# Kernel tuning notes

Hardware: AMD Instinct MI355X
Metric: run time of the kernel (lower is better)

Reference implementation:

```python
import jax, jax.numpy as jnp
import numpy as np

B, N, C = 32, 197, 768
H = 12
D = C // H
NUM_CLASSES = 100
SCALE = D ** -0.5


def setup_inputs() -> dict:
    key = jax.random.key(0)
    ks = jax.random.split(key, 8)
    x = jax.random.normal(ks[0], (B, N, C), dtype=jnp.float32)
    y = jax.random.randint(ks[1], (B,), 0, NUM_CLASSES, dtype=jnp.int32)
    qkv_w = jax.random.normal(ks[2], (3 * C, C), dtype=jnp.float32) * 0.02
    qkv_b = jax.random.normal(ks[3], (3 * C,), dtype=jnp.float32) * 0.02
    proj_w = jax.random.normal(ks[4], (C, C), dtype=jnp.float32) * 0.02
    proj_b = jax.random.normal(ks[5], (C,), dtype=jnp.float32) * 0.02
    mask_attn = jnp.ones((NUM_CLASSES, H, D), jnp.float32) + 0.1 * jax.random.normal(ks[6], (NUM_CLASSES, H, D), dtype=jnp.float32)
    mask_proj = jnp.ones((NUM_CLASSES, C, C), jnp.float32) + 0.1 * jax.random.normal(ks[7], (NUM_CLASSES, C, C), dtype=jnp.float32)
    return {"x": x, "y": y, "qkv_w": qkv_w, "qkv_b": qkv_b,
            "proj_w": proj_w, "proj_b": proj_b,
            "mask_attn": mask_attn, "mask_proj": mask_proj}


def reference(x, y, qkv_w, qkv_b, proj_w, proj_b, mask_attn, mask_proj):
    b, n, c = x.shape
    # qkv projection: (B,N,3C) -> (3,B,H,N,D)
    qkv = (x @ qkv_w.T + qkv_b).reshape(b, n, 3, H, D).transpose(2, 0, 3, 1, 4)
    q, k, v = qkv[0], qkv[1], qkv[2]
    a = jnp.einsum('bhnd,bhmd->bhnm', q * SCALE, k)
    a = jax.nn.softmax(a, axis=-1)  # attn_drop is identity in eval
    o = jnp.einsum('bhnm,bhmd->bhnd', a, v)
    # per-class attention mask: (B,H,1,D)
    o = o * mask_attn[y][:, :, None, :]
    o = o.transpose(0, 2, 1, 3).reshape(b, n, c)
    # per-sample masked projection weight: (B, out, in)
    W = proj_w[None, :, :] * mask_proj[y]
    out = jnp.einsum('bni,boi->bno', o, W) + proj_b[None, None, :]
    return out  # proj_drop is identity in eval
```

## Files before the change

kernel.cpp:

```cpp
#include <hip/hip_runtime.h>

typedef unsigned short u16;
typedef __attribute__((ext_vector_type(8))) short short8;
typedef __attribute__((ext_vector_type(4))) short s16x4;
typedef __attribute__((ext_vector_type(4))) float f32x4;
typedef __attribute__((ext_vector_type(4))) u16 u16x4;

#define GPTR(p) ((const __attribute__((address_space(1))) void*)(p))
#define LPTR(p) ((__attribute__((address_space(3))) void*)(p))

#if __has_builtin(__builtin_amdgcn_mfma_f32_16x16x16bf16_1k)
#define MFMA16x16(a, b, c) __builtin_amdgcn_mfma_f32_16x16x16bf16_1k(a, b, c, 0, 0, 0)
#elif __has_builtin(__builtin_amdgcn_mfma_f32_16x16x16_bf16)
#define MFMA16x16(a, b, c) __builtin_amdgcn_mfma_f32_16x16x16_bf16(a, b, c, 0, 0, 0)
#else
__host__ __device__ static inline f32x4 MFMA16x16_host_stub(s16x4, s16x4, f32x4 c) { return c; }
#define MFMA16x16(a, b, c) MFMA16x16_host_stub(a, b, c)
#endif

__device__ __forceinline__ u16 f2bf(float f) {
    union { float f; unsigned u; } a; a.f = f;
    unsigned r = a.u + 0x7FFFu + ((a.u >> 16) & 1u);
    return (u16)(r >> 16);
}

__global__ __launch_bounds__(256) void cvt_fused_kernel(const float* __restrict__ xin,
                                                        const float* __restrict__ win,
                                                        u16* __restrict__ xout,
                                                        u16* __restrict__ wout) {
    int i = (blockIdx.x * 256 + threadIdx.x) * 4;
    const float* src;
    u16* dst;
    int j;
    if (i < 4841472) {
        src = xin; dst = xout; j = i;
    } else {
        src = win; dst = wout; j = i - 4841472;
    }
    f32x4 v = *(const f32x4*)(src + j);
    u16x4 o;
#pragma unroll
    for (int k = 0; k < 4; ++k) o[k] = f2bf(v[k]);
    *(u16x4*)(dst + j) = o;
}

__global__ __launch_bounds__(512, 2) void qkv_gemm_kernel(
    const u16* __restrict__ A,
    const u16* __restrict__ Bm,
    const float* __restrict__ bias,
    u16* __restrict__ qb, u16* __restrict__ kb, u16* __restrict__ vb) {
    __shared__ __align__(16) u16 As[2][256 * 64];
    __shared__ __align__(16) u16 Bs[2][256 * 64];
    const int tid = threadIdx.x;
    const int w = tid >> 6, l = tid & 63;
    const int wy = w >> 2, wx = w & 3;
    const int dl = l & 15, g4 = l >> 4;
    const int fr = (dl & 7) << 4;

    const int wg = blockIdx.x;
    const int xcd = wg & 7, pos = wg >> 3;
    const int id2 = (xcd < 1 ? xcd * 29 : 29 + (xcd - 1) * 28) + pos;
    const int bm = id2 / 9, bn = id2 % 9;

    f32x4 acc[8][4] = {};

#define QKV_STAGE(bi, kt)                                                                   \
    {                                                                                       \
        _Pragma("unroll")                                                                   \
        for (int cc = 0; cc < 4; ++cc) {                                                    \
            int c = w * 256 + cc * 64 + l;                                                  \
            int row = c >> 3;                                                               \
            int cs = ((c & 7) << 4) ^ ((row & 7) << 4);                                     \
            __builtin_amdgcn_global_load_lds(                                               \
                GPTR((const char*)(A + (size_t)(bm * 256 + row) * 768 + (kt)) + cs),        \
                LPTR((char*)As[bi] + c * 16), 16, 0, 0);                                    \
            __builtin_amdgcn_global_load_lds(                                               \
                GPTR((const char*)(Bm + (size_t)(bn * 256 + row) * 768 + (kt)) + cs),       \
                LPTR((char*)Bs[bi] + c * 16), 16, 0, 0);                                    \
        }                                                                                   \
    }

    QKV_STAGE(0, 0)
    __syncthreads();
    int cur = 0;
#pragma unroll 1
    for (int t = 0; t < 12; ++t) {
        if (t < 11) QKV_STAGE(cur ^ 1, (t + 1) * 64)
#pragma unroll
        for (int s = 0; s < 2; ++s) {
            const int ce = ((s << 6) | (g4 << 4)) ^ fr;
            short8 af[8], bf[4];
#pragma unroll
            for (int mi = 0; mi < 8; ++mi)
                af[mi] = *(const short8*)((const char*)As[cur] + (wy * 128 + mi * 16 + dl) * 128 + ce);
#pragma unroll
            for (int ni = 0; ni < 4; ++ni)
                bf[ni] = *(const short8*)((const char*)Bs[cur] + (wx * 64 + ni * 16 + dl) * 128 + ce);
#pragma unroll
            for (int mi = 0; mi < 8; ++mi)
#pragma unroll
                for (int ni = 0; ni < 4; ++ni)
                    acc[mi][ni] = __builtin_amdgcn_mfma_f32_16x16x32_bf16(af[mi], bf[ni], acc[mi][ni], 0, 0, 0);
        }
        __syncthreads();
        cur ^= 1;
    }
#undef QKV_STAGE

#pragma unroll
    for (int ni = 0; ni < 4; ++ni) {
        int col = bn * 256 + wx * 64 + ni * 16 + dl;
        int s = (col >= 1536) ? 2 : (col >= 768) ? 1 : 0;
        int j = col - s * 768;
        int h = j >> 6, d = j & 63;
        float bv = bias[col];
        u16* dst = (s == 0) ? qb : (s == 1) ? kb : vb;
        float sc = (s == 0) ? 0.125f : 1.0f;
#pragma unroll
        for (int mi = 0; mi < 8; ++mi) {
#pragma unroll
            for (int r = 0; r < 4; ++r) {
                int row = bm * 256 + wy * 128 + mi * 16 + g4 * 4 + r;
                if (row < 6304) {
                    int bi = row / 197;
                    int n = row - bi * 197;
                    dst[((size_t)(bi * 12 + h) * 197 + n) * 64 + d] = f2bf((acc[mi][ni][r] + bv) * sc);
                }
            }
        }
    }
}

#define VPAD 212
__global__ __launch_bounds__(512) void attn_kernel(
    const u16* __restrict__ qg_all, const u16* __restrict__ kg_all, const u16* __restrict__ vg_all,
    const int* __restrict__ y, const float* __restrict__ mask_attn,
    u16* __restrict__ omid) {
    __shared__ __align__(16) u16 Ks[208 * 64];
    __shared__ __align__(16) u16 Vst[64 * VPAD];
    const int bh = blockIdx.x >> 1, half = blockIdx.x & 1;
    const int b = bh / 12, h = bh % 12;
    const int tid = threadIdx.x, w = tid >> 6, l = tid & 63;
    const int dl = l & 15, g = l >> 4;
    const size_t base = (size_t)bh * 197 * 64;
    const u16* qg = qg_all + base;
    const u16* kg = kg_all + base;
    const u16* vg = vg_all + base;
    const short8 zero8 = {0, 0, 0, 0, 0, 0, 0, 0};
    const int ycls = y[b];

    for (int c = tid; c < 208 * 8; c += 512) {
        int row = c >> 3, colb = (c & 7) * 16;
        short8 val = zero8;
        if (row < 197) val = *(const short8*)(kg + row * 64 + (c & 7) * 8);
        int bo = (row * 128 + colb) ^ ((row & 7) << 4);
        *(short8*)((char*)Ks + bo) = val;
    }
    for (int c = tid; c < 208 * 8; c += 512) {
        int row = c >> 3, col = (c & 7) * 8;
        short8 val = zero8;
        if (row < 197) val = *(const short8*)(vg + row * 64 + col);
#pragma unroll
        for (int j = 0; j < 8; ++j) Vst[(col + j) * VPAD + row] = (u16)val[j];
    }
    __syncthreads();

    const int ci_end = half ? 13 : 7;
    for (int ci = half * 7 + w; ci < ci_end; ci += 8) {
        int qrow = ci * 16 + dl;
        const u16* qr = qg + (size_t)qrow * 64 + g * 8;
        short8 q0 = *(const short8*)(qr);
        short8 q1 = *(const short8*)(qr + 32);

        f32x4 sc[13];
#pragma unroll
        for (int jb = 0; jb < 13; ++jb) {
            int krow = jb * 16 + dl;
            int sw = (krow & 7) << 4;
            short8 k0 = *(const short8*)((const char*)Ks + ((krow * 128 + g * 16) ^ sw));
            short8 k1 = *(const short8*)((const char*)Ks + ((krow * 128 + 64 + g * 16) ^ sw));
            f32x4 t = {0.f, 0.f, 0.f, 0.f};
            t = __builtin_amdgcn_mfma_f32_16x16x32_bf16(k0, q0, t, 0, 0, 0);
            t = __builtin_amdgcn_mfma_f32_16x16x32_bf16(k1, q1, t, 0, 0, 0);
            sc[jb] = t;
        }
#pragma unroll
        for (int r = 0; r < 4; ++r)
            if (192 + g * 4 + r >= 197) sc[12][r] = -1e30f;

        float mx = -1e30f;
#pragma unroll
        for (int jb = 0; jb < 13; ++jb)
#pragma unroll
            for (int r = 0; r < 4; ++r) mx = fmaxf(mx, sc[jb][r]);
        mx = fmaxf(mx, __shfl_xor(mx, 16));
        mx = fmaxf(mx, __shfl_xor(mx, 32));
        float ssum = 0.f;
#pragma unroll
        for (int jb = 0; jb < 13; ++jb)
#pragma unroll
            for (int r = 0; r < 4; ++r) {
                float e = __expf(sc[jb][r] - mx);
                sc[jb][r] = e;
                ssum += e;
            }
        ssum += __shfl_xor(ssum, 16);
        ssum += __shfl_xor(ssum, 32);
        float inv = 1.0f / ssum;

        s16x4 pb[13];
#pragma unroll
        for (int jb = 0; jb < 13; ++jb) {
            s16x4 pv;
#pragma unroll
            for (int r = 0; r < 4; ++r) pv[r] = (short)f2bf(sc[jb][r] * inv);
            pb[jb] = pv;
        }

#pragma unroll
        for (int db = 0; db < 4; ++db) {
            f32x4 o = {0.f, 0.f, 0.f, 0.f};
#pragma unroll
            for (int jb = 0; jb < 13; ++jb) {
                s16x4 va = *(const s16x4*)&Vst[(db * 16 + dl) * VPAD + jb * 16 + g * 4];
                o = MFMA16x16(va, pb[jb], o);
            }
            if (qrow < 197) {
                int d = db * 16 + g * 4;
                f32x4 mv = *(const f32x4*)(mask_attn + ((size_t)ycls * 12 + h) * 64 + d);
                u16x4 ov;
#pragma unroll
                for (int r = 0; r < 4; ++r) ov[r] = f2bf(o[r] * mv[r]);
                *(u16x4*)(omid + ((size_t)(b * 256 + qrow)) * 768 + h * 64 + d) = ov;
            }
        }
    }
}

__global__ __launch_bounds__(512, 2) void proj_gemm_kernel(
    const u16* __restrict__ A,
    const float* __restrict__ proj_w,
    const float* __restrict__ mask_proj,
    const int* __restrict__ y,
    const float* __restrict__ bias,
    float* __restrict__ out) {
    __shared__ __align__(16) u16 Ap[2][256 * 64];
    __shared__ __align__(16) u16 Bp[2][128 * 64];
    const int tid = threadIdx.x;
    const int w = tid >> 6, l = tid & 63;
    const int wy = w >> 1, wx = w & 1;
    const int dl = l & 15, g4 = l >> 4;
    const int fr = (dl & 7) << 4;

    const int wg = blockIdx.x;
    const int id2 = (wg & 7) * 24 + (wg >> 3);
    const int b = id2 / 6, bn = id2 % 6;
    const size_t mbase = (size_t)y[b] * 589824;

    const int brow = tid >> 2;
    const int becol = (tid & 3) * 16;
    const int bcb = becol * 2;
    const int bsw = (brow & 7) << 4;

    f32x4 pw[4], pm[4];

#define PROJ_LOADB(kt)                                                              \
    {                                                                               \
        size_t off = (size_t)(bn * 128 + brow) * 768 + (kt) + becol;                \
        _Pragma("unroll")                                                           \
        for (int j = 0; j < 4; ++j) {                                               \
            pw[j] = *(const f32x4*)(proj_w + off + j * 4);                          \
            pm[j] = *(const f32x4*)(mask_proj + mbase + off + j * 4);               \
        }                                                                           \
    }

#define PROJ_WRITEB(bi)                                                             \
    {                                                                               \
        short8 o0, o1;                                                              \
        _Pragma("unroll")                                                           \
        for (int j = 0; j < 4; ++j) {                                               \
            o0[j] = (short)f2bf(pw[0][j] * pm[0][j]);                               \
            o0[4 + j] = (short)f2bf(pw[1][j] * pm[1][j]);                           \
            o1[j] = (short)f2bf(pw[2][j] * pm[2][j]);                               \
            o1[4 + j] = (short)f2bf(pw[3][j] * pm[3][j]);                           \
        }                                                                           \
        char* bp = (char*)Bp[bi] + brow * 128;                                      \
        *(short8*)(bp + (bcb ^ bsw)) = o0;                                          \
        *(short8*)(bp + ((bcb + 16) ^ bsw)) = o1;                                   \
    }

#define PROJ_STAGEA(bi, kt)                                                         \
    {                                                                               \
        _Pragma("unroll")                                                           \
        for (int cc = 0; cc < 4; ++cc) {                                            \
            int c = w * 256 + cc * 64 + l;                                          \
            int row = c >> 3;                                                       \
            int cs = ((c & 7) << 4) ^ ((row & 7) << 4);                             \
            __builtin_amdgcn_global_load_lds(                                       \
                GPTR((const char*)(A + (size_t)(b * 256 + row) * 768 + (kt)) + cs), \
                LPTR((char*)Ap[bi] + c * 16), 16, 0, 0);                            \
        }                                                                           \
    }

    f32x4 acc[4][4] = {};
    PROJ_LOADB(0)
    PROJ_STAGEA(0, 0)
    PROJ_WRITEB(0)
    __syncthreads();
    int cur = 0;
#pragma unroll 1
    for (int t = 0; t < 12; ++t) {
        if (t < 11) {
            PROJ_STAGEA(cur ^ 1, (t + 1) * 64)
            PROJ_LOADB((t + 1) * 64)
        }
#pragma unroll
        for (int s = 0; s < 2; ++s) {
            const int ce = ((s << 6) | (g4 << 4)) ^ fr;
            short8 af[4], bf[4];
#pragma unroll
            for (int mi = 0; mi < 4; ++mi)
                af[mi] = *(const short8*)((const char*)Ap[cur] + (wy * 64 + mi * 16 + dl) * 128 + ce);
#pragma unroll
            for (int ni = 0; ni < 4; ++ni)
                bf[ni] = *(const short8*)((const char*)Bp[cur] + (wx * 64 + ni * 16 + dl) * 128 + ce);
#pragma unroll
            for (int mi = 0; mi < 4; ++mi)
#pragma unroll
                for (int ni = 0; ni < 4; ++ni)
                    acc[mi][ni] = __builtin_amdgcn_mfma_f32_16x16x32_bf16(af[mi], bf[ni], acc[mi][ni], 0, 0, 0);
        }
        if (t < 11) PROJ_WRITEB(cur ^ 1)
        __syncthreads();
        cur ^= 1;
    }

#pragma unroll
    for (int ni = 0; ni < 4; ++ni) {
        int col = bn * 128 + wx * 64 + ni * 16 + dl;
        float bv = bias[col];
#pragma unroll
        for (int mi = 0; mi < 4; ++mi) {
#pragma unroll
            for (int r = 0; r < 4; ++r) {
                int row = wy * 64 + mi * 16 + g4 * 4 + r;
                if (row < 197)
                    out[((size_t)b * 197 + row) * 768 + col] = acc[mi][ni][r] + bv;
            }
        }
    }
#undef PROJ_LOADB
#undef PROJ_WRITEB
#undef PROJ_STAGEA
}

extern "C" void kernel_launch(void* const* d_in, const int* in_sizes, int n_in,
                              void* d_out, int out_size, void* d_ws, size_t ws_size,
                              hipStream_t stream) {
    const float* x = (const float*)d_in[0];
    const int* y = (const int*)d_in[1];
    const float* qkv_w = (const float*)d_in[2];
    const float* qkv_b = (const float*)d_in[3];
    const float* proj_w = (const float*)d_in[4];
    const float* proj_b = (const float*)d_in[5];
    const float* mask_attn = (const float*)d_in[6];
    const float* mask_proj = (const float*)d_in[7];
    float* out = (float*)d_out;

    u16* xb = (u16*)d_ws;
    u16* wqkvb = xb + (size_t)6400 * 768;
    u16* qb = wqkvb + (size_t)2304 * 768;
    u16* kb = qb + (size_t)76288 * 64;
    u16* vb = kb + (size_t)76288 * 64;
    u16* omid = vb + (size_t)76288 * 64;

    cvt_fused_kernel<<<6456, 256, 0, stream>>>(x, qkv_w, xb, wqkvb);
    qkv_gemm_kernel<<<225, 512, 0, stream>>>(xb, wqkvb, qkv_b, qb, kb, vb);
    attn_kernel<<<768, 512, 0, stream>>>(qb, kb, vb, y, mask_attn, omid);
    proj_gemm_kernel<<<192, 512, 0, stream>>>(omid, proj_w, mask_proj, y, proj_b, out);
}
```

Measured before the change: 130.6 us.

## Pipeline QKV GEMM in quarter-stages with fine-grained waits; halve attention block size

```diff
diff --git a/kernel.cpp b/kernel.cpp
--- a/kernel.cpp
+++ b/kernel.cpp
@@ -62,77 +62,118 @@
     const int id2 = (xcd < 1 ? xcd * 29 : 29 + (xcd - 1) * 28) + pos;
     const int bm = id2 / 9, bn = id2 % 9;
 
-    f32x4 acc[8][4] = {};
-
-#define QKV_STAGE(bi, kt)                                                                   \
-    {                                                                                       \
-        _Pragma("unroll")                                                                   \
-        for (int cc = 0; cc < 4; ++cc) {                                                    \
-            int c = w * 256 + cc * 64 + l;                                                  \
-            int row = c >> 3;                                                               \
-            int cs = ((c & 7) << 4) ^ ((row & 7) << 4);                                     \
-            __builtin_amdgcn_global_load_lds(                                               \
-                GPTR((const char*)(A + (size_t)(bm * 256 + row) * 768 + (kt)) + cs),        \
-                LPTR((char*)As[bi] + c * 16), 16, 0, 0);                                    \
-            __builtin_amdgcn_global_load_lds(                                               \
-                GPTR((const char*)(Bm + (size_t)(bn * 256 + row) * 768 + (kt)) + cs),       \
-                LPTR((char*)Bs[bi] + c * 16), 16, 0, 0);                                    \
-        }                                                                                   \
-    }
-
-    QKV_STAGE(0, 0)
-    __syncthreads();
-    int cur = 0;
+#define STG(tau, k)                                                                          \
+    if ((tau) < 12) {                                                                        \
+        const u16* P = ((k) & 1) ? Bm : A;                                                   \
+        const int tb = ((k) & 1) ? bn : bm;                                                  \
+        char* Lb = (char*)(((k) & 1) ? Bs[(tau) & 1] : As[(tau) & 1]);                       \
+        _Pragma("unroll")                                                                    \
+        for (int j = 0; j < 2; ++j) {                                                        \
+            int c = j * 512 + tid;                                                           \
+            int row = (((k) >> 1) << 7) + (c >> 3);                                          \
+            int cs = ((c & 7) << 4) ^ ((row & 7) << 4);                                      \
+            __builtin_amdgcn_global_load_lds(                                                \
+                GPTR((const char*)(P + (size_t)(tb * 256 + row) * 768 + (tau) * 64) + cs),   \
+                LPTR(Lb + row * 128 + ((c & 7) << 4)), 16, 0, 0);                            \
+        }                                                                                    \
+    }
+
+#define RD_A(qm, Tb)                                                                         \
+    _Pragma("unroll")                                                                        \
+    for (int mi = 0; mi < 4; ++mi)                                                           \
+    _Pragma("unroll")                                                                        \
+        for (int s = 0; s < 2; ++s)                                                          \
+            af[mi][s] = *(const short8*)((const char*)As[(Tb)] +                             \
+                ((qm) * 128 + wy * 64 + mi * 16 + dl) * 128 + (((s << 6) | (g4 << 4)) ^ fr));
+
+#define RD_B(qn, Tb)                                                                         \
+    _Pragma("unroll")                                                                        \
+    for (int ni = 0; ni < 2; ++ni)                                                           \
+    _Pragma("unroll")                                                                        \
+        for (int s = 0; s < 2; ++s)                                                          \
+            bf[ni][s] = *(const short8*)((const char*)Bs[(Tb)] +                             \
+                ((qn) * 128 + wx * 32 + ni * 16 + dl) * 128 + (((s << 6) | (g4 << 4)) ^ fr));
+
+#define MM(qm, qn)                                                                           \
+    __builtin_amdgcn_s_setprio(1);                                                           \
+    _Pragma("unroll")                                                                        \
+    for (int s = 0; s < 2; ++s)                                                              \
+    _Pragma("unroll")                                                                        \
+        for (int mi = 0; mi < 4; ++mi)                                                       \
+        _Pragma("unroll")                                                                    \
+            for (int ni = 0; ni < 2; ++ni)                                                   \
+                acc[qm][qn][mi][ni] = __builtin_amdgcn_mfma_f32_16x16x32_bf16(               \
+                    af[mi][s], bf[ni][s], acc[qm][qn][mi][ni], 0, 0, 0);                     \
+    __builtin_amdgcn_s_setprio(0);
+
+#define FENCE asm volatile("" ::: "memory")
+#define VM(n) asm volatile("s_waitcnt vmcnt(" #n ")" ::: "memory")
+#define BAR __builtin_amdgcn_s_barrier()
+
+    f32x4 acc[2][2][4][2] = {};
+    short8 af[4][2], bf[2][2];
+
+    STG(0, 0) STG(0, 1) STG(0, 2) STG(0, 3) STG(1, 0) STG(1, 1)
+
 #pragma unroll 1
-    for (int t = 0; t < 12; ++t) {
-        if (t < 11) QKV_STAGE(cur ^ 1, (t + 1) * 64)
-#pragma unroll
-        for (int s = 0; s < 2; ++s) {
-            const int ce = ((s << 6) | (g4 << 4)) ^ fr;
-            short8 af[8], bf[4];
-#pragma unroll
-            for (int mi = 0; mi < 8; ++mi)
-                af[mi] = *(const short8*)((const char*)As[cur] + (wy * 128 + mi * 16 + dl) * 128 + ce);
-#pragma unroll
-            for (int ni = 0; ni < 4; ++ni)
-                bf[ni] = *(const short8*)((const char*)Bs[cur] + (wx * 64 + ni * 16 + dl) * 128 + ce);
-#pragma unroll
-            for (int mi = 0; mi < 8; ++mi)
-#pragma unroll
-                for (int ni = 0; ni < 4; ++ni)
-                    acc[mi][ni] = __builtin_amdgcn_mfma_f32_16x16x32_bf16(af[mi], bf[ni], acc[mi][ni], 0, 0, 0);
-        }
-        __syncthreads();
-        cur ^= 1;
-    }
-#undef QKV_STAGE
-
-#pragma unroll
-    for (int ni = 0; ni < 4; ++ni) {
-        int col = bn * 256 + wx * 64 + ni * 16 + dl;
-        int s = (col >= 1536) ? 2 : (col >= 768) ? 1 : 0;
-        int j = col - s * 768;
-        int h = j >> 6, d = j & 63;
-        float bv = bias[col];
-        u16* dst = (s == 0) ? qb : (s == 1) ? kb : vb;
-        float sc = (s == 0) ? 0.125f : 1.0f;
-#pragma unroll
-        for (int mi = 0; mi < 8; ++mi) {
-#pragma unroll
-            for (int r = 0; r < 4; ++r) {
-                int row = bm * 256 + wy * 128 + mi * 16 + g4 * 4 + r;
-                if (row < 6304) {
-                    int bi = row / 197;
-                    int n = row - bi * 197;
-                    dst[((size_t)(bi * 12 + h) * 197 + n) * 64 + d] = f2bf((acc[mi][ni][r] + bv) * sc);
-                }
-            }
-        }
-    }
+    for (int T = 0; T < 12; ++T) {
+        const int Tb = T & 1;
+        if (T < 11) { VM(8); } else { VM(4); }
+        BAR; FENCE;
+        RD_A(0, Tb) RD_B(0, Tb)
+        STG(T + 1, 2)
+        MM(0, 0)
+        FENCE; BAR; FENCE;
+        RD_B(1, Tb)
+        STG(T + 1, 3)
+        MM(0, 1)
+        FENCE;
+        if (T < 11) { VM(8); } else { VM(0); }
+        BAR; FENCE;
+        RD_A(1, Tb) RD_B(0, Tb)
+        STG(T + 2, 0)
+        MM(1, 0)
+        FENCE; BAR; FENCE;
+        RD_B(1, Tb)
+        STG(T + 2, 1)
+        MM(1, 1)
+        FENCE;
+    }
+#undef STG
+#undef RD_A
+#undef RD_B
+#undef MM
+
+#pragma unroll
+    for (int qn = 0; qn < 2; ++qn)
+#pragma unroll
+        for (int ni = 0; ni < 2; ++ni) {
+            int col = bn * 256 + qn * 128 + wx * 32 + ni * 16 + dl;
+            int s = (col >= 1536) ? 2 : (col >= 768) ? 1 : 0;
+            int j = col - s * 768;
+            int h = j >> 6, d = j & 63;
+            float bv = bias[col];
+            u16* dst = (s == 0) ? qb : (s == 1) ? kb : vb;
+            float sc = (s == 0) ? 0.125f : 1.0f;
+#pragma unroll
+            for (int qm = 0; qm < 2; ++qm)
+#pragma unroll
+                for (int mi = 0; mi < 4; ++mi)
+#pragma unroll
+                    for (int r = 0; r < 4; ++r) {
+                        int row = bm * 256 + qm * 128 + wy * 64 + mi * 16 + g4 * 4 + r;
+                        if (row < 6304) {
+                            int bi = row / 197;
+                            int n = row - bi * 197;
+                            dst[((size_t)(bi * 12 + h) * 197 + n) * 64 + d] =
+                                f2bf((acc[qm][qn][mi][ni][r] + bv) * sc);
+                        }
+                    }
+        }
 }
 
 #define VPAD 212
-__global__ __launch_bounds__(512) void attn_kernel(
+__global__ __launch_bounds__(256) void attn_kernel(
     const u16* __restrict__ qg_all, const u16* __restrict__ kg_all, const u16* __restrict__ vg_all,
     const int* __restrict__ y, const float* __restrict__ mask_attn,
     u16* __restrict__ omid) {
@@ -149,14 +190,14 @@
     const short8 zero8 = {0, 0, 0, 0, 0, 0, 0, 0};
     const int ycls = y[b];
 
-    for (int c = tid; c < 208 * 8; c += 512) {
+    for (int c = tid; c < 208 * 8; c += 256) {
         int row = c >> 3, colb = (c & 7) * 16;
         short8 val = zero8;
         if (row < 197) val = *(const short8*)(kg + row * 64 + (c & 7) * 8);
         int bo = (row * 128 + colb) ^ ((row & 7) << 4);
         *(short8*)((char*)Ks + bo) = val;
     }
-    for (int c = tid; c < 208 * 8; c += 512) {
+    for (int c = tid; c < 208 * 8; c += 256) {
         int row = c >> 3, col = (c & 7) * 8;
         short8 val = zero8;
         if (row < 197) val = *(const short8*)(vg + row * 64 + col);
@@ -166,7 +207,7 @@
     __syncthreads();
 
     const int ci_end = half ? 13 : 7;
-    for (int ci = half * 7 + w; ci < ci_end; ci += 8) {
+    for (int ci = half * 7 + w; ci < ci_end; ci += 4) {
         int qrow = ci * 16 + dl;
         const u16* qr = qg + (size_t)qrow * 64 + g * 8;
         short8 q0 = *(const short8*)(qr);
@@ -376,6 +417,6 @@
 
     cvt_fused_kernel<<<6456, 256, 0, stream>>>(x, qkv_w, xb, wqkvb);
     qkv_gemm_kernel<<<225, 512, 0, stream>>>(xb, wqkvb, qkv_b, qb, kb, vb);
-    attn_kernel<<<768, 512, 0, stream>>>(qb, kb, vb, y, mask_attn, omid);
+    attn_kernel<<<768, 256, 0, stream>>>(qb, kb, vb, y, mask_attn, omid);
     proj_gemm_kernel<<<192, 512, 0, stream>>>(omid, proj_w, mask_proj, y, proj_b, out);
 }
```

Measured after the change: 127.2 us. 2.7% less time.
